# Kernel tuning notes

Measured on AMD Instinct MI355X. Metric: run time of the kernel, lower is better.

The kernel has to match this reference:

```python
import jax, jax.numpy as jnp
import numpy as np

K = 3            # spline kernel_size per pseudo-coord dim (dim=2 -> K*K=9 weights)
FILTERS = [64, 64, 64]
N_OUT = 10


def _spline_basis(u):
    # u: [B,N,N,2], open degree-1 B-spline basis on pseudo-coords in [0,1]
    v = u * (K - 1)
    i0 = jnp.clip(jnp.floor(v), 0.0, K - 2)
    f = v - i0                                  # fractional part in [0,1]
    i0 = i0.astype(jnp.int32)
    b = (1.0 - f)[..., None] * jax.nn.one_hot(i0, K, dtype=u.dtype) \
        + f[..., None] * jax.nn.one_hot(i0 + 1, K, dtype=u.dtype)   # [B,N,N,2,K]
    basis = b[..., 0, :, None] * b[..., 1, None, :]                  # [B,N,N,K,K]
    return basis.reshape(u.shape[0], u.shape[1], u.shape[2], K * K)  # [B,N,N,9]


def _spline_conv(h, basis_masked, deg, w, root, bias):
    # h: [B,N,Cin]; basis_masked: [B,N,N,9]; w: [9,Cin,Cout]
    hw = jnp.einsum('bmc,kcf->bmkf', h, w)                 # per-kernel transformed feats
    agg = jnp.einsum('bnmk,bmkf->bnf', basis_masked, hw) / deg   # mean neighbor aggregation
    return agg + h @ root + bias


def setup_inputs() -> dict:
    key = jax.random.key(0)
    B, N, C = 32, 512, 128   # C = in_features + 18
    ks = jax.random.split(key, 16)
    x = jax.random.normal(ks[0], (B, N, C), jnp.float32)
    coord = jax.random.uniform(ks[1], (B, N, 2), jnp.float32)
    adj = (jax.random.uniform(ks[2], (B, N, N), jnp.float32) < 0.06).astype(jnp.float32)
    adj = adj * (1.0 - jnp.eye(N, dtype=jnp.float32))  # no self-loops; root weight handles self
    inp = {"x": x, "coord": coord, "adj": adj}
    cin = C
    for l, f in enumerate(FILTERS):
        inp[f"w{l}"] = jax.random.normal(ks[3 + 3 * l], (K * K, cin, f), jnp.float32) / np.float32(np.sqrt(cin * K * K))
        inp[f"root{l}"] = jax.random.normal(ks[4 + 3 * l], (cin, f), jnp.float32) / np.float32(np.sqrt(cin))
        inp[f"b{l}"] = jnp.zeros((f,), jnp.float32)
        cin = f
    inp["fc_w"] = jax.random.normal(ks[13], (FILTERS[-1], N_OUT), jnp.float32) / np.float32(np.sqrt(FILTERS[-1]))
    inp["fc_b"] = jnp.zeros((N_OUT,), jnp.float32)
    return inp


def reference(x, coord, adj, w0, root0, b0, w1, root1, b1, w2, root2, b2, fc_w, fc_b):
    # get_monet_coord: relative 2D offsets of connected nodes, mapped to [0,1]
    u = (coord[:, None, :, :] - coord[:, :, None, :] + 1.0) * 0.5     # [B,N,N,2]
    basis = _spline_basis(u) * adj[..., None]                          # mask to edges
    deg = jnp.clip(jnp.sum(adj, axis=-1, keepdims=True), 1.0, None)   # [B,N,1]
    h = x
    for w, r, b in ((w0, root0, b0), (w1, root1, b1), (w2, root2, b2)):
        h = jax.nn.relu(_spline_conv(h, basis, deg, w, r, b))
    g = jnp.max(h, axis=1)          # global max-pool over nodes -> [B, 64]
    return g @ fc_w + fc_b          # dropout is an inference no-op -> [B, 10]
```

## Files before the change

kernel.cpp:

```cpp
#include <hip/hip_runtime.h>


#define B_   32
#define N_   512
#define F_   64
#define CAP  128

typedef float f32x4 __attribute__((ext_vector_type(4)));
typedef _Float16 f16x8 __attribute__((ext_vector_type(8)));
typedef _Float16 f16x2 __attribute__((ext_vector_type(2)));

__global__ __launch_bounds__(512) void preprocess_kernel(
    const float* __restrict__ adj, const float* __restrict__ coord,
    float4* __restrict__ edge, int4* __restrict__ cnt4,
    float* __restrict__ deginv, unsigned int* __restrict__ gmax) {
  int row = blockIdx.x;
  int b = row >> 9;
  int tid = threadIdx.x;
  int lane = tid & 63, wave = tid >> 6;
  if (row < B_ * F_ && tid == 0) gmax[row] = 0u;
  __shared__ int wc[8][4];
  float a = adj[(size_t)row * N_ + tid];
  bool flag = (a != 0.0f);
  float cxn = coord[(size_t)row * 2 + 0];
  float cyn = coord[(size_t)row * 2 + 1];
  float cxm = coord[(size_t)(b * N_ + tid) * 2 + 0];
  float cym = coord[(size_t)(b * N_ + tid) * 2 + 1];
  float vx = (cxm - cxn + 1.0f);
  float vy = (cym - cyn + 1.0f);
  float i0x = fminf(fmaxf(floorf(vx), 0.0f), 1.0f);
  float i0y = fminf(fmaxf(floorf(vy), 0.0f), 1.0f);
  float fx = vx - i0x, fy = vy - i0y;
  int quad = (int)i0x + 2 * (int)i0y;
  unsigned long long bq0 = __ballot(flag && quad == 0);
  unsigned long long bq1 = __ballot(flag && quad == 1);
  unsigned long long bq2 = __ballot(flag && quad == 2);
  unsigned long long bq3 = __ballot(flag && quad == 3);
  if (lane == 0) {
    wc[wave][0] = __popcll(bq0); wc[wave][1] = __popcll(bq1);
    wc[wave][2] = __popcll(bq2); wc[wave][3] = __popcll(bq3);
  }
  __syncthreads();
  int qt0 = 0, qt1 = 0, qt2 = 0, qt3 = 0;
  #pragma unroll
  for (int w2 = 0; w2 < 8; ++w2) {
    qt0 += wc[w2][0]; qt1 += wc[w2][1]; qt2 += wc[w2][2]; qt3 += wc[w2][3];
  }
  if (flag) {
    int off = 0;
    if (quad > 0) off += qt0;
    if (quad > 1) off += qt1;
    if (quad > 2) off += qt2;
    #pragma unroll
    for (int w2 = 0; w2 < 8; ++w2)
      if (w2 < wave) off += wc[w2][quad];
    unsigned long long myb = (quad == 0) ? bq0 : (quad == 1) ? bq1
                           : (quad == 2) ? bq2 : bq3;
    off += __popcll(myb & ((1ULL << lane) - 1ULL));
    if (off < CAP)
      edge[(size_t)row * CAP + off] =
          make_float4(__int_as_float(tid), fx, fy, 1.0f);
  }
  if (tid == 0) {
    int rem = CAP;
    int c0 = min(qt0, rem); rem -= c0;
    int c1 = min(qt1, rem); rem -= c1;
    int c2 = min(qt2, rem); rem -= c2;
    int c3 = min(qt3, rem);
    cnt4[row] = make_int4(c0, c1, c2, c3);
    int total = qt0 + qt1 + qt2 + qt3;
    deginv[row] = 1.0f / (float)(total > 0 ? total : 1);
  }
}

__global__ void convx16_kernel(const float* __restrict__ x, _Float16* __restrict__ hx) {
  int idx = blockIdx.x * blockDim.x + threadIdx.x;
  if (idx >= B_ * N_ * 32) return;
  float4 v = ((const float4*)x)[idx];
  f16x2 p0, p1;
  p0[0] = (_Float16)v.x; p0[1] = (_Float16)v.y;
  p1[0] = (_Float16)v.z; p1[1] = (_Float16)v.w;
  uint2 u;
  u.x = __builtin_bit_cast(unsigned, p0);
  u.y = __builtin_bit_cast(unsigned, p1);
  ((uint2*)hx)[idx] = u;
}

__global__ void packw3_kernel(
    const float* __restrict__ w0, const float* __restrict__ root0,
    const float* __restrict__ w1, const float* __restrict__ root1,
    const float* __restrict__ w2, const float* __restrict__ root2,
    _Float16* __restrict__ wt0, _Float16* __restrict__ wt1,
    _Float16* __restrict__ wt2) {
  int idx = blockIdx.x * blockDim.x + threadIdx.x;
  const int S0 = 64 * 1280, S1 = 64 * 640;
  const float *w, *root; _Float16* wt; int KP, CIN, r;
  if (idx < S0)            { w = w0; root = root0; wt = wt0; KP = 1280; CIN = 128; r = idx; }
  else if (idx < S0 + S1)  { w = w1; root = root1; wt = wt1; KP = 640;  CIN = 64;  r = idx - S0; }
  else if (idx < S0 + 2*S1){ w = w2; root = root2; wt = wt2; KP = 640;  CIN = 64;  r = idx - S0 - S1; }
  else return;
  int f = r / KP, k = r - f * KP;
  int ks = k / CIN, c = k - ks * CIN;
  float v = (ks < 9) ? w[((size_t)ks * CIN + c) * F_ + f]
                     : root[(size_t)c * F_ + f];
  wt[(size_t)f * KP + k] = (_Float16)v;
}

template<int CH>
__global__ __launch_bounds__(256, 6) void gather_kernel(
    const _Float16* __restrict__ hsrc,
    const float4* __restrict__ edge, const int4* __restrict__ cnt4,
    const float* __restrict__ deginv,
    _Float16* __restrict__ sp) {
  const int CIN = 64 * CH, KP = 10 * CIN;
  __shared__ float4 esh[4][CAP];
  int wave = threadIdx.x >> 6, lane = threadIdx.x & 63;
  int xcd = blockIdx.x & 7;
  int j = blockIdx.x >> 3;
  int b = xcd * 4 + (j >> 7);
  int n = ((j & 127) << 2) + wave;
  int row = (b << 9) + n;
  int4 c4 = cnt4[row];
  int e1 = c4.x, e2 = e1 + c4.y, e3 = e2 + c4.z, e4 = e3 + c4.w;
  size_t ebase = (size_t)row * CAP;
  for (int i = lane; i < e4; i += 64)
    esh[wave][i] = edge[ebase + i];
  float di = deginv[row];
  const _Float16* hb = hsrc + (size_t)b * N_ * CIN + lane * CH;

  float acc[3][3][CH];
  #pragma unroll
  for (int kx = 0; kx < 3; ++kx)
    #pragma unroll
    for (int ky = 0; ky < 3; ++ky)
      #pragma unroll
      for (int c = 0; c < CH; ++c) acc[kx][ky][c] = 0.0f;

#define EDGE_BODY(E, KX, KY) {                                        \
    float4 er = esh[wave][E];                                         \
    int m = __float_as_int(er.x);                                     \
    float hv[CH];                                                     \
    if (CH == 1) {                                                    \
      hv[0] = (float)hb[(size_t)m * 64];                              \
    } else {                                                          \
      unsigned u = *(const unsigned*)&hb[(size_t)m * 128];            \
      f16x2 hp = __builtin_bit_cast(f16x2, u);                        \
      hv[0] = (float)hp[0]; hv[CH - 1] = (float)hp[1];                \
    }                                                                 \
    float fx = er.y, fy = er.z;                                       \
    float gx = 1.0f - fx, gy = 1.0f - fy;                             \
    float w00 = gx * gy, w01 = gx * fy, w10 = fx * gy, w11 = fx * fy; \
    _Pragma("unroll")                                                 \
    for (int c = 0; c < CH; ++c) {                                    \
      acc[KX][KY][c]         += w00 * hv[c];                          \
      acc[KX][KY + 1][c]     += w01 * hv[c];                          \
      acc[KX + 1][KY][c]     += w10 * hv[c];                          \
      acc[KX + 1][KY + 1][c] += w11 * hv[c];                          \
    } }

  #pragma unroll 4
  for (int e = 0; e < e1; ++e) EDGE_BODY(e, 0, 0)
  #pragma unroll 4
  for (int e = e1; e < e2; ++e) EDGE_BODY(e, 1, 0)
  #pragma unroll 4
  for (int e = e2; e < e3; ++e) EDGE_BODY(e, 0, 1)
  #pragma unroll 4
  for (int e = e3; e < e4; ++e) EDGE_BODY(e, 1, 1)
#undef EDGE_BODY

  _Float16* sr = sp + (size_t)row * KP + lane * CH;
  #pragma unroll
  for (int kx = 0; kx < 3; ++kx)
    #pragma unroll
    for (int ky = 0; ky < 3; ++ky) {
      int k = kx * 3 + ky;
      if (CH == 1) {
        sr[(size_t)k * CIN] = (_Float16)(acc[kx][ky][0] * di);
      } else {
        f16x2 p;
        p[0] = (_Float16)(acc[kx][ky][0] * di);
        p[1] = (_Float16)(acc[kx][ky][CH - 1] * di);
        *(f16x2*)&sr[(size_t)k * CIN] = p;
      }
    }
  if (CH == 1) {
    sr[(size_t)9 * CIN] = hb[(size_t)n * 64];
  } else {
    *(unsigned*)&sr[(size_t)9 * CIN] = *(const unsigned*)&hb[(size_t)n * 128];
  }
}

#define GBK  64
#define GLDK 72
__global__ __launch_bounds__(256) void gemm_s_kernel(
    const _Float16* __restrict__ A, const _Float16* __restrict__ Wt,
    const float* __restrict__ bias, _Float16* __restrict__ hout,
    unsigned int* __restrict__ gmax, int KP) {
  __shared__ __attribute__((aligned(16))) _Float16 As[2][64 * GLDK];
  __shared__ __attribute__((aligned(16))) _Float16 Ws[2][64 * GLDK];
  int bm = blockIdx.x << 6;
  int tid = threadIdx.x, wave = tid >> 6, lane = tid & 63;
  int lr = lane & 15, quad = lane >> 4;
  int srow = tid >> 3, sck = (tid & 7) * 8;
  const size_t aoff = (size_t)(bm + srow) * KP + sck;
  const size_t woff = (size_t)srow * KP + sck;

  f32x4 acc[4] = {};
  {
    *(float4*)&As[0][srow * GLDK + sck]        = *(const float4*)&A[aoff];
    *(float4*)&As[0][(srow + 32) * GLDK + sck] = *(const float4*)&A[aoff + (size_t)32 * KP];
    *(float4*)&Ws[0][srow * GLDK + sck]        = *(const float4*)&Wt[woff];
    *(float4*)&Ws[0][(srow + 32) * GLDK + sck] = *(const float4*)&Wt[woff + (size_t)32 * KP];
  }
  int S = KP / GBK, cur = 0;
  float4 pa0, pa1, pw0, pw1;
  for (int s = 0; s < S; ++s) {
    if (s + 1 < S) {
      int k0 = (s + 1) * GBK;
      pa0 = *(const float4*)&A[aoff + k0];
      pa1 = *(const float4*)&A[aoff + (size_t)32 * KP + k0];
      pw0 = *(const float4*)&Wt[woff + k0];
      pw1 = *(const float4*)&Wt[woff + (size_t)32 * KP + k0];
    }
    __syncthreads();
    #pragma unroll
    for (int kk = 0; kk < GBK; kk += 32) {
      f16x8 af = *(const f16x8*)&As[cur][(16 * wave + lr) * GLDK + kk + quad * 8];
      #pragma unroll
      for (int j = 0; j < 4; ++j) {
        f16x8 bf = *(const f16x8*)&Ws[cur][(16 * j + lr) * GLDK + kk + quad * 8];
        acc[j] = __builtin_amdgcn_mfma_f32_16x16x32_f16(af, bf, acc[j], 0, 0, 0);
      }
    }
    if (s + 1 < S) {
      int nb = cur ^ 1;
      *(float4*)&As[nb][srow * GLDK + sck]        = pa0;
      *(float4*)&As[nb][(srow + 32) * GLDK + sck] = pa1;
      *(float4*)&Ws[nb][srow * GLDK + sck]        = pw0;
      *(float4*)&Ws[nb][(srow + 32) * GLDK + sck] = pw1;
    }
    cur ^= 1;
  }
  int b = bm >> 9;
  #pragma unroll
  for (int j = 0; j < 4; ++j) {
    int f = 16 * j + lr;
    float bs = bias[f];
    float vmax = 0.0f;
    #pragma unroll
    for (int r = 0; r < 4; ++r) {
      int m = bm + (wave << 4) + (quad << 2) + r;
      float v = fmaxf(acc[j][r] + bs, 0.0f);
      if (hout) hout[(size_t)m * F_ + f] = (_Float16)v;
      vmax = fmaxf(vmax, v);
    }
    if (gmax) atomicMax(&gmax[(b << 6) + f], __float_as_uint(vmax));
  }
}

__global__ __launch_bounds__(64) void fc_kernel(
    const float* __restrict__ g, const float* __restrict__ fcw,
    const float* __restrict__ fcb, float* __restrict__ out) {
  int b = blockIdx.x;
  int f = threadIdx.x;
  __shared__ float gs[64];
  gs[f] = g[b * F_ + f];
  __syncthreads();
  if (f < 10) {
    float s = fcb[f];
    #pragma unroll
    for (int c = 0; c < 64; ++c) s += gs[c] * fcw[c * 10 + f];
    out[b * 10 + f] = s;
  }
}

extern "C" void kernel_launch(void* const* d_in, const int* in_sizes, int n_in,
                              void* d_out, int out_size, void* d_ws, size_t ws_size,
                              hipStream_t stream) {
  const float* x     = (const float*)d_in[0];
  const float* coord = (const float*)d_in[1];
  const float* adj   = (const float*)d_in[2];
  const float* w0    = (const float*)d_in[3];
  const float* root0 = (const float*)d_in[4];
  const float* b0    = (const float*)d_in[5];
  const float* w1    = (const float*)d_in[6];
  const float* root1 = (const float*)d_in[7];
  const float* b1    = (const float*)d_in[8];
  const float* w2    = (const float*)d_in[9];
  const float* root2 = (const float*)d_in[10];
  const float* b2    = (const float*)d_in[11];
  const float* fcw   = (const float*)d_in[12];
  const float* fcb   = (const float*)d_in[13];
  float* out = (float*)d_out;

  char* ws = (char*)d_ws;
  size_t off = 0;
  auto alloc = [&](size_t bytes) {
    void* p = ws + off;
    off = (off + bytes + 255) & ~(size_t)255;
    return p;
  };
  const int R = B_ * N_;
  float4* edge    = (float4*)alloc((size_t)R * CAP * 16);
  int4*   cnt4    = (int4*)  alloc((size_t)R * 16);
  float*  deginv  = (float*) alloc((size_t)R * 4);
  _Float16* hx    = (_Float16*)alloc((size_t)R * 128 * 2);
  _Float16* wt0   = (_Float16*)alloc((size_t)64 * 1280 * 2);
  _Float16* wt1   = (_Float16*)alloc((size_t)64 * 640 * 2);
  _Float16* wt2   = (_Float16*)alloc((size_t)64 * 640 * 2);
  _Float16* sp    = (_Float16*)alloc((size_t)R * 1280 * 2);
  _Float16* hA    = (_Float16*)alloc((size_t)R * 64 * 2);
  _Float16* hB    = (_Float16*)alloc((size_t)R * 64 * 2);
  unsigned int* gmax = (unsigned int*)alloc((size_t)B_ * F_ * 4);

  preprocess_kernel<<<R, 512, 0, stream>>>(adj, coord, edge, cnt4, deginv, gmax);
  convx16_kernel<<<(R * 32 + 255) / 256, 256, 0, stream>>>(x, hx);
  packw3_kernel<<<(64 * (1280 + 640 + 640) + 255) / 256, 256, 0, stream>>>(
      w0, root0, w1, root1, w2, root2, wt0, wt1, wt2);

  gather_kernel<2><<<R / 4, 256, 0, stream>>>(hx, edge, cnt4, deginv, sp);
  gemm_s_kernel<<<R / 64, 256, 0, stream>>>(sp, wt0, b0, hA, nullptr, 1280);

  gather_kernel<1><<<R / 4, 256, 0, stream>>>(hA, edge, cnt4, deginv, sp);
  gemm_s_kernel<<<R / 64, 256, 0, stream>>>(sp, wt1, b1, hB, nullptr, 640);

  gather_kernel<1><<<R / 4, 256, 0, stream>>>(hB, edge, cnt4, deginv, sp);
  gemm_s_kernel<<<R / 64, 256, 0, stream>>>(sp, wt2, b2, nullptr, gmax, 640);

  fc_kernel<<<B_, 64, 0, stream>>>((const float*)gmax, fcw, fcb, out);
}
```

Measured before the change: 239.1 us.

## Fuse gather and GEMM per layer, keeping spline features in LDS

Merges the per-layer gather kernel and the MFMA GEMM kernel into one kernel. Each block gathers a tile of 16 or 32 rows into shared memory, then multiplies it with the packed weights read straight from global memory. This removes the large fp16 intermediate buffer (R x 1280) and its write and re-read, plus three kernel launches. In exchange each block is larger and sequential, occupancy drops (launch bounds 3), and the weight operand is no longer staged in LDS.

```diff
diff --git a/kernel.cpp b/kernel.cpp
--- a/kernel.cpp
+++ b/kernel.cpp
@@ -106,35 +106,37 @@
   wt[(size_t)f * KP + k] = (_Float16)v;
 }
 
-template<int CH>
-__global__ __launch_bounds__(256, 6) void gather_kernel(
+template<int CH, int MT>
+__global__ __launch_bounds__(256, 3) void fused_layer_kernel(
     const _Float16* __restrict__ hsrc,
+    const _Float16* __restrict__ Wt,
+    const float* __restrict__ bias,
     const float4* __restrict__ edge, const int4* __restrict__ cnt4,
     const float* __restrict__ deginv,
-    _Float16* __restrict__ sp) {
-  const int CIN = 64 * CH, KP = 10 * CIN;
+    _Float16* __restrict__ hout,
+    unsigned int* __restrict__ gmax) {
+  const int CIN = 64 * CH, K = 10 * CIN, SLD = K + 8;
+  __shared__ __attribute__((aligned(16))) _Float16 st[MT * SLD];
   __shared__ float4 esh[4][CAP];
-  int wave = threadIdx.x >> 6, lane = threadIdx.x & 63;
-  int xcd = blockIdx.x & 7;
-  int j = blockIdx.x >> 3;
-  int b = xcd * 4 + (j >> 7);
-  int n = ((j & 127) << 2) + wave;
-  int row = (b << 9) + n;
-  int4 c4 = cnt4[row];
-  int e1 = c4.x, e2 = e1 + c4.y, e3 = e2 + c4.z, e4 = e3 + c4.w;
-  size_t ebase = (size_t)row * CAP;
-  for (int i = lane; i < e4; i += 64)
-    esh[wave][i] = edge[ebase + i];
-  float di = deginv[row];
+  int tid = threadIdx.x, wave = tid >> 6, lane = tid & 63;
+  const int BPB = 512 / MT;
+  int xcd = blockIdx.x & 7, j = blockIdx.x >> 3;
+  int b = xcd * 4 + j / BPB;
+  int tile = j & (BPB - 1);
+  int rowbase = (b << 9) + tile * MT;
   const _Float16* hb = hsrc + (size_t)b * N_ * CIN + lane * CH;
 
-  float acc[3][3][CH];
-  #pragma unroll
-  for (int kx = 0; kx < 3; ++kx)
-    #pragma unroll
-    for (int ky = 0; ky < 3; ++ky)
-      #pragma unroll
-      for (int c = 0; c < CH; ++c) acc[kx][ky][c] = 0.0f;
+  const int RW = MT / 4;
+  for (int rr = 0; rr < RW; ++rr) {
+    int tr = wave * RW + rr;
+    int row = rowbase + tr;
+    int4 c4 = cnt4[row];
+    int e1 = c4.x, e2 = e1 + c4.y, e3 = e2 + c4.z, e4 = e3 + c4.w;
+    size_t ebase = (size_t)row * CAP;
+    for (int i = lane; i < e4; i += 64)
+      esh[wave][i] = edge[ebase + i];
+    float di = deginv[row];
+    float acc[3][3][CH] = {};
 
 #define EDGE_BODY(E, KX, KY) {                                        \
     float4 er = esh[wave][E];                                         \
@@ -158,99 +160,63 @@
       acc[KX + 1][KY + 1][c] += w11 * hv[c];                          \
     } }
 
+    #pragma unroll 4
+    for (int e = 0; e < e1; ++e) EDGE_BODY(e, 0, 0)
+    #pragma unroll 4
+    for (int e = e1; e < e2; ++e) EDGE_BODY(e, 1, 0)
+    #pragma unroll 4
+    for (int e = e2; e < e3; ++e) EDGE_BODY(e, 0, 1)
+    #pragma unroll 4
+    for (int e = e3; e < e4; ++e) EDGE_BODY(e, 1, 1)
+#undef EDGE_BODY
+
+    _Float16* sr = st + tr * SLD + lane * CH;
+    #pragma unroll
+    for (int kx = 0; kx < 3; ++kx)
+      #pragma unroll
+      for (int ky = 0; ky < 3; ++ky) {
+        int k = kx * 3 + ky;
+        if (CH == 1) {
+          sr[k * CIN] = (_Float16)(acc[kx][ky][0] * di);
+        } else {
+          f16x2 p;
+          p[0] = (_Float16)(acc[kx][ky][0] * di);
+          p[1] = (_Float16)(acc[kx][ky][CH - 1] * di);
+          *(f16x2*)&sr[k * CIN] = p;
+        }
+      }
+    if (CH == 1) {
+      sr[9 * CIN] = hb[(size_t)(row - (b << 9)) * 64];
+    } else {
+      *(unsigned*)&sr[9 * CIN] = *(const unsigned*)&hb[(size_t)(row - (b << 9)) * 128];
+    }
+  }
+  __syncthreads();
+
+  const int CT = MT / 16;
+  int lr = lane & 15, quad = lane >> 4;
+  f32x4 acc2[CT];
+  #pragma unroll
+  for (int ct = 0; ct < CT; ++ct) acc2[ct] = (f32x4){0.f, 0.f, 0.f, 0.f};
+  const _Float16* wrow = Wt + (size_t)(wave * 16 + lr) * K + quad * 8;
   #pragma unroll 4
-  for (int e = 0; e < e1; ++e) EDGE_BODY(e, 0, 0)
-  #pragma unroll 4
-  for (int e = e1; e < e2; ++e) EDGE_BODY(e, 1, 0)
-  #pragma unroll 4
-  for (int e = e2; e < e3; ++e) EDGE_BODY(e, 0, 1)
-  #pragma unroll 4
-  for (int e = e3; e < e4; ++e) EDGE_BODY(e, 1, 1)
-#undef EDGE_BODY
-
-  _Float16* sr = sp + (size_t)row * KP + lane * CH;
+  for (int ks = 0; ks < K; ks += 32) {
+    f16x8 bf = *(const f16x8*)(wrow + ks);
+    #pragma unroll
+    for (int ct = 0; ct < CT; ++ct) {
+      f16x8 af = *(const f16x8*)&st[(ct * 16 + lr) * SLD + ks + quad * 8];
+      acc2[ct] = __builtin_amdgcn_mfma_f32_16x16x32_f16(af, bf, acc2[ct], 0, 0, 0);
+    }
+  }
+  int f = wave * 16 + lr;
+  float bs = bias[f];
   #pragma unroll
-  for (int kx = 0; kx < 3; ++kx)
-    #pragma unroll
-    for (int ky = 0; ky < 3; ++ky) {
-      int k = kx * 3 + ky;
-      if (CH == 1) {
-        sr[(size_t)k * CIN] = (_Float16)(acc[kx][ky][0] * di);
-      } else {
-        f16x2 p;
-        p[0] = (_Float16)(acc[kx][ky][0] * di);
-        p[1] = (_Float16)(acc[kx][ky][CH - 1] * di);
-        *(f16x2*)&sr[(size_t)k * CIN] = p;
-      }
-    }
-  if (CH == 1) {
-    sr[(size_t)9 * CIN] = hb[(size_t)n * 64];
-  } else {
-    *(unsigned*)&sr[(size_t)9 * CIN] = *(const unsigned*)&hb[(size_t)n * 128];
-  }
-}
-
-#define GBK  64
-#define GLDK 72
-__global__ __launch_bounds__(256) void gemm_s_kernel(
-    const _Float16* __restrict__ A, const _Float16* __restrict__ Wt,
-    const float* __restrict__ bias, _Float16* __restrict__ hout,
-    unsigned int* __restrict__ gmax, int KP) {
-  __shared__ __attribute__((aligned(16))) _Float16 As[2][64 * GLDK];
-  __shared__ __attribute__((aligned(16))) _Float16 Ws[2][64 * GLDK];
-  int bm = blockIdx.x << 6;
-  int tid = threadIdx.x, wave = tid >> 6, lane = tid & 63;
-  int lr = lane & 15, quad = lane >> 4;
-  int srow = tid >> 3, sck = (tid & 7) * 8;
-  const size_t aoff = (size_t)(bm + srow) * KP + sck;
-  const size_t woff = (size_t)srow * KP + sck;
-
-  f32x4 acc[4] = {};
-  {
-    *(float4*)&As[0][srow * GLDK + sck]        = *(const float4*)&A[aoff];
-    *(float4*)&As[0][(srow + 32) * GLDK + sck] = *(const float4*)&A[aoff + (size_t)32 * KP];
-    *(float4*)&Ws[0][srow * GLDK + sck]        = *(const float4*)&Wt[woff];
-    *(float4*)&Ws[0][(srow + 32) * GLDK + sck] = *(const float4*)&Wt[woff + (size_t)32 * KP];
-  }
-  int S = KP / GBK, cur = 0;
-  float4 pa0, pa1, pw0, pw1;
-  for (int s = 0; s < S; ++s) {
-    if (s + 1 < S) {
-      int k0 = (s + 1) * GBK;
-      pa0 = *(const float4*)&A[aoff + k0];
-      pa1 = *(const float4*)&A[aoff + (size_t)32 * KP + k0];
-      pw0 = *(const float4*)&Wt[woff + k0];
-      pw1 = *(const float4*)&Wt[woff + (size_t)32 * KP + k0];
-    }
-    __syncthreads();
-    #pragma unroll
-    for (int kk = 0; kk < GBK; kk += 32) {
-      f16x8 af = *(const f16x8*)&As[cur][(16 * wave + lr) * GLDK + kk + quad * 8];
-      #pragma unroll
-      for (int j = 0; j < 4; ++j) {
-        f16x8 bf = *(const f16x8*)&Ws[cur][(16 * j + lr) * GLDK + kk + quad * 8];
-        acc[j] = __builtin_amdgcn_mfma_f32_16x16x32_f16(af, bf, acc[j], 0, 0, 0);
-      }
-    }
-    if (s + 1 < S) {
-      int nb = cur ^ 1;
-      *(float4*)&As[nb][srow * GLDK + sck]        = pa0;
-      *(float4*)&As[nb][(srow + 32) * GLDK + sck] = pa1;
-      *(float4*)&Ws[nb][srow * GLDK + sck]        = pw0;
-      *(float4*)&Ws[nb][(srow + 32) * GLDK + sck] = pw1;
-    }
-    cur ^= 1;
-  }
-  int b = bm >> 9;
-  #pragma unroll
-  for (int j = 0; j < 4; ++j) {
-    int f = 16 * j + lr;
-    float bs = bias[f];
+  for (int ct = 0; ct < CT; ++ct) {
     float vmax = 0.0f;
     #pragma unroll
     for (int r = 0; r < 4; ++r) {
-      int m = bm + (wave << 4) + (quad << 2) + r;
-      float v = fmaxf(acc[j][r] + bs, 0.0f);
+      int m = rowbase + ct * 16 + (quad << 2) + r;
+      float v = fmaxf(acc2[ct][r] + bs, 0.0f);
       if (hout) hout[(size_t)m * F_ + f] = (_Float16)v;
       vmax = fmaxf(vmax, v);
     }
@@ -308,7 +274,6 @@
   _Float16* wt0   = (_Float16*)alloc((size_t)64 * 1280 * 2);
   _Float16* wt1   = (_Float16*)alloc((size_t)64 * 640 * 2);
   _Float16* wt2   = (_Float16*)alloc((size_t)64 * 640 * 2);
-  _Float16* sp    = (_Float16*)alloc((size_t)R * 1280 * 2);
   _Float16* hA    = (_Float16*)alloc((size_t)R * 64 * 2);
   _Float16* hB    = (_Float16*)alloc((size_t)R * 64 * 2);
   unsigned int* gmax = (unsigned int*)alloc((size_t)B_ * F_ * 4);
@@ -318,14 +283,12 @@
   packw3_kernel<<<(64 * (1280 + 640 + 640) + 255) / 256, 256, 0, stream>>>(
       w0, root0, w1, root1, w2, root2, wt0, wt1, wt2);
 
-  gather_kernel<2><<<R / 4, 256, 0, stream>>>(hx, edge, cnt4, deginv, sp);
-  gemm_s_kernel<<<R / 64, 256, 0, stream>>>(sp, wt0, b0, hA, nullptr, 1280);
-
-  gather_kernel<1><<<R / 4, 256, 0, stream>>>(hA, edge, cnt4, deginv, sp);
-  gemm_s_kernel<<<R / 64, 256, 0, stream>>>(sp, wt1, b1, hB, nullptr, 640);
-
-  gather_kernel<1><<<R / 4, 256, 0, stream>>>(hB, edge, cnt4, deginv, sp);
-  gemm_s_kernel<<<R / 64, 256, 0, stream>>>(sp, wt2, b2, nullptr, gmax, 640);
+  fused_layer_kernel<2, 16><<<R / 16, 256, 0, stream>>>(
+      hx, wt0, b0, edge, cnt4, deginv, hA, nullptr);
+  fused_layer_kernel<1, 32><<<R / 32, 256, 0, stream>>>(
+      hA, wt1, b1, edge, cnt4, deginv, hB, nullptr);
+  fused_layer_kernel<1, 32><<<R / 32, 256, 0, stream>>>(
+      hB, wt2, b2, edge, cnt4, deginv, nullptr, gmax);
 
   fc_kernel<<<B_, 64, 0, stream>>>((const float*)gmax, fcw, fcb, out);
 }
```

After: 263.1 us. +10.0%, slower.
